# Kernel tuning notes

Hardware: AMD Instinct MI355X
Metric: run time of the kernel (lower is better)

Reference implementation:

```python
import jax, jax.numpy as jnp
import numpy as np

DIM = 64  # per-head dim used for the sqrt scale


def setup_inputs() -> dict:
    key = jax.random.key(0)
    kq, kk, kv, ke, kf = jax.random.split(key, 5)
    B, N, d, k = 32, 4096, 64, 256
    Q = jax.random.normal(kq, (B, N, d), dtype=jnp.float32)
    K = jax.random.normal(kk, (B, N, d), dtype=jnp.float32)
    V = jax.random.normal(kv, (B, N, d), dtype=jnp.float32)
    E = jax.random.normal(ke, (N, k), dtype=jnp.float32) * (1.0 / np.sqrt(N))
    F = jax.random.normal(kf, (N, k), dtype=jnp.float32) * (1.0 / np.sqrt(N))
    return {"Q": Q, "K": K, "V": V, "E": E, "F": F}


def reference(Q, K, V, E, F):
    # Linformer head: K^T E -> [B,d,k]; Q (K^T E) / sqrt(d) -> [B,N,k]
    K_proj = jnp.einsum('bnd,nk->bdk', K, E)          # low-rank key projection
    scores = jnp.einsum('bnd,bdk->bnk', Q, K_proj) / jnp.sqrt(jnp.float32(DIM))
    P_bar = jax.nn.softmax(scores, axis=2)            # [B,N,k]
    # (V^T F)^T -> [B,k,d]
    V_proj = jnp.einsum('bnd,nk->bkd', V, F)
    return jnp.einsum('bnk,bkd->bnd', P_bar, V_proj)  # [B,N,d]
```

## Files before the change

### kernel.cpp

```cpp
#include <hip/hip_runtime.h>
#include <hip/hip_bf16.h>

#define BB 32
#define NN 4096
#define DDIM 64
#define KKR 256

typedef __attribute__((ext_vector_type(8)))  short bf16x8;
typedef __attribute__((ext_vector_type(16))) float f32x16;
typedef __attribute__((ext_vector_type(4)))  float f32x4;

static __device__ inline unsigned short f2bf(float x) {
  union { float f; unsigned u; } v; v.f = x;
  unsigned r = (v.u + 0x7FFFu + ((v.u >> 16) & 1u)) >> 16;
  return (unsigned short)r;
}

__global__ __launch_bounds__(256) void pass0_kernel(
    const float* __restrict__ Q, const float* __restrict__ K,
    const float* __restrict__ V, const float* __restrict__ E,
    const float* __restrict__ F,
    unsigned short* __restrict__ Qb, unsigned short* __restrict__ KT,
    unsigned short* __restrict__ VT, unsigned short* __restrict__ ET,
    unsigned short* __restrict__ FT)
{
  __shared__ unsigned short T[64 * 72];
  const int id = blockIdx.x;
  const int t  = threadIdx.x;

  if (id < 4608) {
    const float* src; unsigned short* dst; int srcStride, row0, col0;
    if (id < 2048) {
      int b = id >> 6, nt = id & 63;
      src = K + (long)b * NN * DDIM; dst = KT + (long)b * DDIM * NN;
      srcStride = 64; row0 = nt * 64; col0 = 0;
    } else if (id < 4096) {
      int i2 = id - 2048; int b = i2 >> 6, nt = i2 & 63;
      src = V + (long)b * NN * DDIM; dst = VT + (long)b * DDIM * NN;
      srcStride = 64; row0 = nt * 64; col0 = 0;
    } else if (id < 4352) {
      int i2 = id - 4096; int nt = i2 >> 2, ct = i2 & 3;
      src = E; dst = ET; srcStride = 256; row0 = nt * 64; col0 = ct * 64;
    } else {
      int i2 = id - 4352; int nt = i2 >> 2, ct = i2 & 3;
      src = F; dst = FT; srcStride = 256; row0 = nt * 64; col0 = ct * 64;
    }
    const int r  = t >> 2;
    const int cq = t & 3;
    const float* sp = src + (long)(row0 + r) * srcStride + col0 + cq * 16;
    float4 v0 = *(const float4*)(sp + 0);
    float4 v1 = *(const float4*)(sp + 4);
    float4 v2 = *(const float4*)(sp + 8);
    float4 v3 = *(const float4*)(sp + 12);
    const int cb = cq * 16;
    T[(cb + 0)  * 72 + r] = f2bf(v0.x);  T[(cb + 1)  * 72 + r] = f2bf(v0.y);
    T[(cb + 2)  * 72 + r] = f2bf(v0.z);  T[(cb + 3)  * 72 + r] = f2bf(v0.w);
    T[(cb + 4)  * 72 + r] = f2bf(v1.x);  T[(cb + 5)  * 72 + r] = f2bf(v1.y);
    T[(cb + 6)  * 72 + r] = f2bf(v1.z);  T[(cb + 7)  * 72 + r] = f2bf(v1.w);
    T[(cb + 8)  * 72 + r] = f2bf(v2.x);  T[(cb + 9)  * 72 + r] = f2bf(v2.y);
    T[(cb + 10) * 72 + r] = f2bf(v2.z);  T[(cb + 11) * 72 + r] = f2bf(v2.w);
    T[(cb + 12) * 72 + r] = f2bf(v3.x);  T[(cb + 13) * 72 + r] = f2bf(v3.y);
    T[(cb + 14) * 72 + r] = f2bf(v3.z);  T[(cb + 15) * 72 + r] = f2bf(v3.w);
    __syncthreads();
    const int cf = t >> 2;
    const int no = (t & 3) * 16;
    bf16x8 o0 = *(const bf16x8*)&T[cf * 72 + no];
    bf16x8 o1 = *(const bf16x8*)&T[cf * 72 + no + 8];
    unsigned short* dp = dst + (long)(col0 + cf) * NN + row0 + no;
    *(bf16x8*)dp       = o0;
    *(bf16x8*)(dp + 8) = o1;
  } else {
    const long base = (long)(id - 4608) * 4096 + t * 16;
    float4 a = *(const float4*)(Q + base + 0);
    float4 b = *(const float4*)(Q + base + 4);
    float4 c = *(const float4*)(Q + base + 8);
    float4 d = *(const float4*)(Q + base + 12);
    unsigned short o[16];
    o[0]=f2bf(a.x); o[1]=f2bf(a.y); o[2]=f2bf(a.z); o[3]=f2bf(a.w);
    o[4]=f2bf(b.x); o[5]=f2bf(b.y); o[6]=f2bf(b.z); o[7]=f2bf(b.w);
    o[8]=f2bf(c.x); o[9]=f2bf(c.y); o[10]=f2bf(c.z); o[11]=f2bf(c.w);
    o[12]=f2bf(d.x); o[13]=f2bf(d.y); o[14]=f2bf(d.z); o[15]=f2bf(d.w);
    *(bf16x8*)(Qb + base)     = *(const bf16x8*)&o[0];
    *(bf16x8*)(Qb + base + 8) = *(const bf16x8*)&o[8];
  }
}

__global__ __launch_bounds__(256, 2) void proj_gemm(
    const unsigned short* __restrict__ KT, const unsigned short* __restrict__ VT,
    const unsigned short* __restrict__ ET, const unsigned short* __restrict__ FT,
    float* __restrict__ KpA, float* __restrict__ VpA)
{
  extern __shared__ unsigned short sm[];
  const int blk = blockIdx.x;
  const int chunk = blk & 7, mat = (blk >> 3) & 1, b = blk >> 4;
  const int t = threadIdx.x, w = t >> 6, l = t & 63, h = l >> 5, lr = l & 31;

  const unsigned short *Ag, *Bg; int M; float* Cg;
  if (mat == 0) { Ag = ET; Bg = KT + (long)b * DDIM * NN; M = 256; Cg = KpA + b * 16384; }
  else          { Ag = VT + (long)b * DDIM * NN; Bg = FT; M = 64;  Cg = VpA + b * 16384; }
  const int mt0 = (mat == 0) ? 2 * w : 0;
  const int nt0 = (mat == 0) ? 0 : 2 * w;

  f32x16 acc[2][2];
#pragma unroll
  for (int i = 0; i < 2; ++i)
#pragma unroll
    for (int j = 0; j < 2; ++j)
#pragma unroll
      for (int q = 0; q < 16; ++q) acc[i][j][q] = 0.f;

  const int n0 = chunk * 512;
  for (int stg = 0; stg < 8; ++stg) {
    const int nb = n0 + stg * 64;
    __syncthreads();
#pragma unroll
    for (int i = 0; i < 10; ++i) {
      int c = i * 256 + t;
      int row = c >> 3, off = c & 7;
      const unsigned short* g =
          (row < M ? Ag + (long)row * NN : Bg + (long)(row - M) * NN) + nb + off * 8;
      *(bf16x8*)&sm[row * 72 + off * 8] = *(const bf16x8*)g;
    }
    __syncthreads();
#pragma unroll
    for (int kk = 0; kk < 4; ++kk) {
      bf16x8 a0 = *(const bf16x8*)&sm[(mt0 * 32 + lr) * 72 + kk * 16 + h * 8];
      bf16x8 a1 = *(const bf16x8*)&sm[((mt0 + 1) * 32 + lr) * 72 + kk * 16 + h * 8];
      bf16x8 b0 = *(const bf16x8*)&sm[(M + nt0 * 32 + lr) * 72 + kk * 16 + h * 8];
      bf16x8 b1 = *(const bf16x8*)&sm[(M + (nt0 + 1) * 32 + lr) * 72 + kk * 16 + h * 8];
      acc[0][0] = __builtin_amdgcn_mfma_f32_32x32x16_bf16(a0, b0, acc[0][0], 0, 0, 0);
      acc[0][1] = __builtin_amdgcn_mfma_f32_32x32x16_bf16(a0, b1, acc[0][1], 0, 0, 0);
      acc[1][0] = __builtin_amdgcn_mfma_f32_32x32x16_bf16(a1, b0, acc[1][0], 0, 0, 0);
      acc[1][1] = __builtin_amdgcn_mfma_f32_32x32x16_bf16(a1, b1, acc[1][1], 0, 0, 0);
    }
  }
#pragma unroll
  for (int mt = 0; mt < 2; ++mt)
#pragma unroll
    for (int nt = 0; nt < 2; ++nt)
#pragma unroll
      for (int i = 0; i < 16; ++i) {
        int row = (mt0 + mt) * 32 + (i & 3) + 8 * (i >> 2) + 4 * h;
        int col = (nt0 + nt) * 32 + lr;
        int idx = (mat == 0) ? row * 64 + col : row * 256 + col;
        unsafeAtomicAdd(&Cg[idx], acc[mt][nt][i]);
      }
}

__global__ __launch_bounds__(256) void cvt_kernel(
    const float* __restrict__ src, unsigned short* __restrict__ dst)
{
  const long i = ((long)blockIdx.x * 256 + threadIdx.x) * 8;
  float4 a = *(const float4*)(src + i);
  float4 b = *(const float4*)(src + i + 4);
  unsigned short o[8];
  o[0]=f2bf(a.x); o[1]=f2bf(a.y); o[2]=f2bf(a.z); o[3]=f2bf(a.w);
  o[4]=f2bf(b.x); o[5]=f2bf(b.y); o[6]=f2bf(b.z); o[7]=f2bf(b.w);
  *(bf16x8*)(dst + i) = *(const bf16x8*)&o[0];
}

__global__ __launch_bounds__(256, 2) void attn2_kernel(
    const unsigned short* __restrict__ Qb, const unsigned short* __restrict__ Kpb,
    const unsigned short* __restrict__ Vpb, float* __restrict__ Og)
{
  extern __shared__ char smraw[];
  unsigned short* P = (unsigned short*)smraw;
  float* scr = (float*)(smraw + 65536);
  float* red = (float*)(smraw + 65536 + 8192);

  const int blk = blockIdx.x;
  const int b = blk >> 5, rg = blk & 31;
  const int t = threadIdx.x, w = t >> 6, l = t & 63, h = l >> 5, lr = l & 31;
  const int rh = w >> 1, ch = w & 1;

  const unsigned short* Qbase = Qb + ((long)b * NN + rg * 128) * 64;
  bf16x8 A[2][4];
#pragma unroll
  for (int rt = 0; rt < 2; ++rt)
#pragma unroll
    for (int kk = 0; kk < 4; ++kk)
      A[rt][kk] = *(const bf16x8*)(Qbase + (long)(rh * 64 + rt * 32 + lr) * 64 + kk * 16 + h * 8);

  const unsigned short* Kp = Kpb + (long)b * 16384;
  f32x16 acc[2][4];
#pragma unroll
  for (int rt = 0; rt < 2; ++rt)
#pragma unroll
    for (int ct = 0; ct < 4; ++ct)
#pragma unroll
      for (int q = 0; q < 16; ++q) acc[rt][ct][q] = 0.f;

  bf16x8 Bf[4], Bn[4];
#pragma unroll
  for (int ct = 0; ct < 4; ++ct)
    Bf[ct] = *(const bf16x8*)(Kp + (long)(ch * 128 + ct * 32 + lr) * 64 + h * 8);
#pragma unroll
  for (int kk = 0; kk < 4; ++kk) {
    if (kk < 3) {
#pragma unroll
      for (int ct = 0; ct < 4; ++ct)
        Bn[ct] = *(const bf16x8*)(Kp + (long)(ch * 128 + ct * 32 + lr) * 64 + (kk + 1) * 16 + h * 8);
    }
#pragma unroll
    for (int ct = 0; ct < 4; ++ct) {
      acc[0][ct] = __builtin_amdgcn_mfma_f32_32x32x16_bf16(A[0][kk], Bf[ct], acc[0][ct], 0, 0, 0);
      acc[1][ct] = __builtin_amdgcn_mfma_f32_32x32x16_bf16(A[1][kk], Bf[ct], acc[1][ct], 0, 0, 0);
    }
#pragma unroll
    for (int ct = 0; ct < 4; ++ct) Bf[ct] = Bn[ct];
  }

#pragma unroll
  for (int rt = 0; rt < 2; ++rt)
#pragma unroll
    for (int ct = 0; ct < 4; ++ct)
#pragma unroll
      for (int q = 0; q < 16; ++q)
        acc[rt][ct][q] = __expf(acc[rt][ct][q] * 0.125f);

  float ps[2][16];
#pragma unroll
  for (int rt = 0; rt < 2; ++rt)
#pragma unroll
    for (int q = 0; q < 16; ++q)
      ps[rt][q] = (acc[rt][0][q] + acc[rt][1][q]) + (acc[rt][2][q] + acc[rt][3][q]);
#pragma unroll
  for (int rt = 0; rt < 2; ++rt)
#pragma unroll
    for (int q = 0; q < 16; ++q) {
      ps[rt][q] += __shfl_xor(ps[rt][q], 8);
      ps[rt][q] += __shfl_xor(ps[rt][q], 16);
    }
  if (((l >> 3) & 3) == 0) {
#pragma unroll
    for (int rt = 0; rt < 2; ++rt)
#pragma unroll
      for (int q = 0; q < 16; ++q) {
        int rowL = (q & 3) + 8 * (q >> 2) + 4 * h;
        scr[w * 512 + (rt * 32 + rowL) * 8 + (l & 7)] = ps[rt][q];
      }
  }
  {
    const float* p = &scr[w * 512 + l * 8];
    f32x4 x = *(const f32x4*)p, y = *(const f32x4*)(p + 4);
    float s = (x[0] + x[1]) + (x[2] + x[3]) + (y[0] + y[1]) + (y[2] + y[3]);
    red[ch * 128 + rh * 64 + l] = s;
  }

#pragma unroll
  for (int rt = 0; rt < 2; ++rt)
#pragma unroll
    for (int ct = 0; ct < 4; ++ct)
#pragma unroll
      for (int q = 0; q < 16; ++q) {
        int rowL = rh * 64 + rt * 32 + (q & 3) + 8 * (q >> 2) + 4 * h;
        int col  = ch * 128 + ct * 32 + lr;
        int chk  = (col >> 3) ^ (rowL & 7);
        P[rowL * 256 + chk * 8 + (col & 7)] = f2bf(acc[rt][ct][q]);
      }
  __syncthreads();

  const unsigned short* Vp = Vpb + (long)b * 16384;
  f32x16 o[2];
#pragma unroll
  for (int rt = 0; rt < 2; ++rt)
#pragma unroll
    for (int q = 0; q < 16; ++q) o[rt][q] = 0.f;

#pragma unroll
  for (int kk = 0; kk < 16; ++kk) {
    bf16x8 Bv = *(const bf16x8*)(Vp + (long)(ch * 32 + lr) * 256 + kk * 16 + h * 8);
    bf16x8 Ap[2];
#pragma unroll
    for (int rt = 0; rt < 2; ++rt) {
      int rowL = rh * 64 + rt * 32 + lr;
      int col  = kk * 16 + h * 8;
      int chk  = (col >> 3) ^ (rowL & 7);
      Ap[rt] = *(const bf16x8*)&P[rowL * 256 + chk * 8];
    }
    o[0] = __builtin_amdgcn_mfma_f32_32x32x16_bf16(Ap[0], Bv, o[0], 0, 0, 0);
    o[1] = __builtin_amdgcn_mfma_f32_32x32x16_bf16(Ap[1], Bv, o[1], 0, 0, 0);
  }

#pragma unroll
  for (int rt = 0; rt < 2; ++rt)
#pragma unroll
    for (int ig = 0; ig < 4; ++ig) {
      int r0 = rh * 64 + rt * 32 + ig * 8 + 4 * h;
      f32x4 l0 = *(const f32x4*)&red[r0];
      f32x4 l1 = *(const f32x4*)&red[128 + r0];
#pragma unroll
      for (int j = 0; j < 4; ++j) {
        float val = o[rt][ig * 4 + j] / (l0[j] + l1[j]);
        Og[((long)b * NN + rg * 128 + r0 + j) * 64 + ch * 32 + lr] = val;
      }
    }
}

extern "C" void kernel_launch(void* const* d_in, const int* in_sizes, int n_in,
                              void* d_out, int out_size, void* d_ws, size_t ws_size,
                              hipStream_t stream) {
  const float* Q = (const float*)d_in[0];
  const float* K = (const float*)d_in[1];
  const float* V = (const float*)d_in[2];
  const float* E = (const float*)d_in[3];
  const float* F = (const float*)d_in[4];
  float* out = (float*)d_out;

  char* ws = (char*)d_ws;
  float*          KpA = (float*)(ws);
  float*          VpA = (float*)(ws + (2l << 20));
  unsigned short* Kpb = (unsigned short*)(ws + (4l << 20));
  unsigned short* Vpb = (unsigned short*)(ws + (5l << 20));
  unsigned short* Qb  = (unsigned short*)(ws + (6l << 20));
  unsigned short* KT  = (unsigned short*)(ws + (22l << 20));
  unsigned short* VT  = (unsigned short*)(ws + (38l << 20));
  unsigned short* ET  = (unsigned short*)(ws + (54l << 20));
  unsigned short* FT  = (unsigned short*)(ws + (56l << 20));

  hipMemsetAsync(d_ws, 0, (size_t)4 << 20, stream);

  pass0_kernel<<<dim3(6656), dim3(256), 0, stream>>>(Q, K, V, E, F, Qb, KT, VT, ET, FT);

  hipFuncSetAttribute((const void*)proj_gemm,
                      hipFuncAttributeMaxDynamicSharedMemorySize, 46080);
  proj_gemm<<<dim3(512), dim3(256), 46080, stream>>>(KT, VT, ET, FT, KpA, VpA);

  cvt_kernel<<<dim3(512), dim3(256), 0, stream>>>(KpA, Kpb);

  hipFuncSetAttribute((const void*)attn2_kernel,
                      hipFuncAttributeMaxDynamicSharedMemorySize, 74752);
  attn2_kernel<<<dim3(1024), dim3(256), 74752, stream>>>(Qb, Kpb, Vpb, out);
}
```

Before: 230.3 us.

## Fuse Q conversion into attention, replace atomics with partial-sum reduction

Drops the separate Q fp32->bf16 pass and converts Q directly when loading it in the attention kernel, removing a full write and re-read of a Qb buffer. The projection GEMM now uses 4 chunks with plain stores of per-chunk partials, and a new reduce_cvt kernel sums them and converts both Kp and Vp to bf16. This removes the workspace memset and the atomics. pass0's transpose now uses strided scalar loads and direct stores instead of an LDS-staged transpose, which may coalesce worse. exp is switched to exp2 with a prescaled constant and the final division to a reciprocal multiply.

```diff
diff --git a/kernel.cpp b/kernel.cpp
--- a/kernel.cpp
+++ b/kernel.cpp
@@ -17,87 +17,62 @@
 }
 
 __global__ __launch_bounds__(256) void pass0_kernel(
-    const float* __restrict__ Q, const float* __restrict__ K,
-    const float* __restrict__ V, const float* __restrict__ E,
-    const float* __restrict__ F,
-    unsigned short* __restrict__ Qb, unsigned short* __restrict__ KT,
-    unsigned short* __restrict__ VT, unsigned short* __restrict__ ET,
-    unsigned short* __restrict__ FT)
+    const float* __restrict__ K, const float* __restrict__ V,
+    const float* __restrict__ E, const float* __restrict__ F,
+    unsigned short* __restrict__ KT, unsigned short* __restrict__ VT,
+    unsigned short* __restrict__ ET, unsigned short* __restrict__ FT)
 {
-  __shared__ unsigned short T[64 * 72];
   const int id = blockIdx.x;
   const int t  = threadIdx.x;
-
-  if (id < 4608) {
-    const float* src; unsigned short* dst; int srcStride, row0, col0;
-    if (id < 2048) {
-      int b = id >> 6, nt = id & 63;
-      src = K + (long)b * NN * DDIM; dst = KT + (long)b * DDIM * NN;
-      srcStride = 64; row0 = nt * 64; col0 = 0;
-    } else if (id < 4096) {
-      int i2 = id - 2048; int b = i2 >> 6, nt = i2 & 63;
-      src = V + (long)b * NN * DDIM; dst = VT + (long)b * DDIM * NN;
-      srcStride = 64; row0 = nt * 64; col0 = 0;
-    } else if (id < 4352) {
-      int i2 = id - 4096; int nt = i2 >> 2, ct = i2 & 3;
-      src = E; dst = ET; srcStride = 256; row0 = nt * 64; col0 = ct * 64;
-    } else {
-      int i2 = id - 4352; int nt = i2 >> 2, ct = i2 & 3;
-      src = F; dst = FT; srcStride = 256; row0 = nt * 64; col0 = ct * 64;
-    }
-    const int r  = t >> 2;
-    const int cq = t & 3;
-    const float* sp = src + (long)(row0 + r) * srcStride + col0 + cq * 16;
-    float4 v0 = *(const float4*)(sp + 0);
-    float4 v1 = *(const float4*)(sp + 4);
-    float4 v2 = *(const float4*)(sp + 8);
-    float4 v3 = *(const float4*)(sp + 12);
-    const int cb = cq * 16;
-    T[(cb + 0)  * 72 + r] = f2bf(v0.x);  T[(cb + 1)  * 72 + r] = f2bf(v0.y);
-    T[(cb + 2)  * 72 + r] = f2bf(v0.z);  T[(cb + 3)  * 72 + r] = f2bf(v0.w);
-    T[(cb + 4)  * 72 + r] = f2bf(v1.x);  T[(cb + 5)  * 72 + r] = f2bf(v1.y);
-    T[(cb + 6)  * 72 + r] = f2bf(v1.z);  T[(cb + 7)  * 72 + r] = f2bf(v1.w);
-    T[(cb + 8)  * 72 + r] = f2bf(v2.x);  T[(cb + 9)  * 72 + r] = f2bf(v2.y);
-    T[(cb + 10) * 72 + r] = f2bf(v2.z);  T[(cb + 11) * 72 + r] = f2bf(v2.w);
-    T[(cb + 12) * 72 + r] = f2bf(v3.x);  T[(cb + 13) * 72 + r] = f2bf(v3.y);
-    T[(cb + 14) * 72 + r] = f2bf(v3.z);  T[(cb + 15) * 72 + r] = f2bf(v3.w);
-    __syncthreads();
-    const int cf = t >> 2;
-    const int no = (t & 3) * 16;
-    bf16x8 o0 = *(const bf16x8*)&T[cf * 72 + no];
-    bf16x8 o1 = *(const bf16x8*)&T[cf * 72 + no + 8];
-    unsigned short* dp = dst + (long)(col0 + cf) * NN + row0 + no;
-    *(bf16x8*)dp       = o0;
-    *(bf16x8*)(dp + 8) = o1;
+  const float* src; unsigned short* dst; int stride, n0, col0;
+  if (id < 2048) {
+    int b = id >> 6, nt = id & 63;
+    src = K + (long)b * NN * DDIM; dst = KT + (long)b * DDIM * NN;
+    stride = 64; n0 = nt * 64; col0 = 0;
+  } else if (id < 4096) {
+    int i2 = id - 2048; int b = i2 >> 6, nt = i2 & 63;
+    src = V + (long)b * NN * DDIM; dst = VT + (long)b * DDIM * NN;
+    stride = 64; n0 = nt * 64; col0 = 0;
+  } else if (id < 4352) {
+    int i2 = id - 4096; int nt = i2 >> 2, ct = i2 & 3;
+    src = E; dst = ET; stride = 256; n0 = nt * 64; col0 = ct * 64;
   } else {
-    const long base = (long)(id - 4608) * 4096 + t * 16;
-    float4 a = *(const float4*)(Q + base + 0);
-    float4 b = *(const float4*)(Q + base + 4);
-    float4 c = *(const float4*)(Q + base + 8);
-    float4 d = *(const float4*)(Q + base + 12);
-    unsigned short o[16];
-    o[0]=f2bf(a.x); o[1]=f2bf(a.y); o[2]=f2bf(a.z); o[3]=f2bf(a.w);
-    o[4]=f2bf(b.x); o[5]=f2bf(b.y); o[6]=f2bf(b.z); o[7]=f2bf(b.w);
-    o[8]=f2bf(c.x); o[9]=f2bf(c.y); o[10]=f2bf(c.z); o[11]=f2bf(c.w);
-    o[12]=f2bf(d.x); o[13]=f2bf(d.y); o[14]=f2bf(d.z); o[15]=f2bf(d.w);
-    *(bf16x8*)(Qb + base)     = *(const bf16x8*)&o[0];
-    *(bf16x8*)(Qb + base + 8) = *(const bf16x8*)&o[8];
-  }
+    int i2 = id - 4352; int nt = i2 >> 2, ct = i2 & 3;
+    src = F; dst = FT; stride = 256; n0 = nt * 64; col0 = ct * 64;
+  }
+  const int c = t & 63;
+  const int q = t >> 6;
+  const float* sp = src + (long)(n0 + q * 16) * stride + col0 + c;
+  float v[16];
+#pragma unroll
+  for (int j = 0; j < 16; ++j) v[j] = sp[(long)j * stride];
+  unsigned short o[16];
+#pragma unroll
+  for (int j = 0; j < 16; ++j) o[j] = f2bf(v[j]);
+  unsigned short* dp = dst + (long)(col0 + c) * NN + n0 + q * 16;
+#pragma unroll
+  for (int j4 = 0; j4 < 4; ++j4)
+    *(ushort4*)(dp + j4 * 4) = *(const ushort4*)&o[j4 * 4];
 }
 
 __global__ __launch_bounds__(256, 2) void proj_gemm(
     const unsigned short* __restrict__ KT, const unsigned short* __restrict__ VT,
     const unsigned short* __restrict__ ET, const unsigned short* __restrict__ FT,
-    float* __restrict__ KpA, float* __restrict__ VpA)
+    float* __restrict__ KpP, float* __restrict__ VpP)
 {
   extern __shared__ unsigned short sm[];
   const int blk = blockIdx.x;
-  const int chunk = blk & 7, mat = (blk >> 3) & 1, b = blk >> 4;
+  const int chunk = blk & 3, mat = (blk >> 2) & 1, b = blk >> 3;
   const int t = threadIdx.x, w = t >> 6, l = t & 63, h = l >> 5, lr = l & 31;
 
   const unsigned short *Ag, *Bg; int M; float* Cg;
-  if (mat == 0) { Ag = ET; Bg = KT + (long)b * DDIM * NN; M = 256; Cg = KpA + b * 16384; }
-  else          { Ag = VT + (long)b * DDIM * NN; Bg = FT; M = 64;  Cg = VpA + b * 16384; }
+  if (mat == 0) {
+    Ag = ET; Bg = KT + (long)b * DDIM * NN; M = 256;
+    Cg = KpP + (long)chunk * (BB * 16384) + b * 16384;
+  } else {
+    Ag = VT + (long)b * DDIM * NN; Bg = FT; M = 64;
+    Cg = VpP + (long)chunk * (BB * 16384) + b * 16384;
+  }
   const int mt0 = (mat == 0) ? 2 * w : 0;
   const int nt0 = (mat == 0) ? 0 : 2 * w;
 
@@ -109,14 +84,14 @@
 #pragma unroll
       for (int q = 0; q < 16; ++q) acc[i][j][q] = 0.f;
 
-  const int n0 = chunk * 512;
-  for (int stg = 0; stg < 8; ++stg) {
+  const int n0 = chunk * 1024;
+  for (int stg = 0; stg < 16; ++stg) {
     const int nb = n0 + stg * 64;
     __syncthreads();
 #pragma unroll
     for (int i = 0; i < 10; ++i) {
-      int c = i * 256 + t;
-      int row = c >> 3, off = c & 7;
+      int cidx = i * 256 + t;
+      int row = cidx >> 3, off = cidx & 7;
       const unsigned short* g =
           (row < M ? Ag + (long)row * NN : Bg + (long)(row - M) * NN) + nb + off * 8;
       *(bf16x8*)&sm[row * 72 + off * 8] = *(const bf16x8*)g;
@@ -143,24 +118,36 @@
         int row = (mt0 + mt) * 32 + (i & 3) + 8 * (i >> 2) + 4 * h;
         int col = (nt0 + nt) * 32 + lr;
         int idx = (mat == 0) ? row * 64 + col : row * 256 + col;
-        unsafeAtomicAdd(&Cg[idx], acc[mt][nt][i]);
+        Cg[idx] = acc[mt][nt][i];
       }
 }
 
-__global__ __launch_bounds__(256) void cvt_kernel(
-    const float* __restrict__ src, unsigned short* __restrict__ dst)
+__global__ __launch_bounds__(256) void reduce_cvt(
+    const float* __restrict__ KpP, const float* __restrict__ VpP,
+    unsigned short* __restrict__ Kpb, unsigned short* __restrict__ Vpb)
 {
-  const long i = ((long)blockIdx.x * 256 + threadIdx.x) * 8;
-  float4 a = *(const float4*)(src + i);
-  float4 b = *(const float4*)(src + i + 4);
+  const int blk = blockIdx.x;
+  const float* src = (blk < 256) ? KpP : VpP;
+  unsigned short* dst = (blk < 256) ? Kpb : Vpb;
+  const long i = (long)(blk & 255) * 2048 + threadIdx.x * 8;
+  float a[8];
+#pragma unroll
+  for (int j = 0; j < 8; ++j) a[j] = 0.f;
+#pragma unroll
+  for (int cch = 0; cch < 4; ++cch) {
+    const float4 p0 = *(const float4*)(src + (long)cch * (BB * 16384) + i);
+    const float4 p1 = *(const float4*)(src + (long)cch * (BB * 16384) + i + 4);
+    a[0] += p0.x; a[1] += p0.y; a[2] += p0.z; a[3] += p0.w;
+    a[4] += p1.x; a[5] += p1.y; a[6] += p1.z; a[7] += p1.w;
+  }
   unsigned short o[8];
-  o[0]=f2bf(a.x); o[1]=f2bf(a.y); o[2]=f2bf(a.z); o[3]=f2bf(a.w);
-  o[4]=f2bf(b.x); o[5]=f2bf(b.y); o[6]=f2bf(b.z); o[7]=f2bf(b.w);
+#pragma unroll
+  for (int j = 0; j < 8; ++j) o[j] = f2bf(a[j]);
   *(bf16x8*)(dst + i) = *(const bf16x8*)&o[0];
 }
 
 __global__ __launch_bounds__(256, 2) void attn2_kernel(
-    const unsigned short* __restrict__ Qb, const unsigned short* __restrict__ Kpb,
+    const float* __restrict__ Qg, const unsigned short* __restrict__ Kpb,
     const unsigned short* __restrict__ Vpb, float* __restrict__ Og)
 {
   extern __shared__ char smraw[];
@@ -173,13 +160,20 @@
   const int t = threadIdx.x, w = t >> 6, l = t & 63, h = l >> 5, lr = l & 31;
   const int rh = w >> 1, ch = w & 1;
 
-  const unsigned short* Qbase = Qb + ((long)b * NN + rg * 128) * 64;
+  const float* Qbase = Qg + ((long)b * NN + rg * 128) * 64;
   bf16x8 A[2][4];
 #pragma unroll
   for (int rt = 0; rt < 2; ++rt)
 #pragma unroll
-    for (int kk = 0; kk < 4; ++kk)
-      A[rt][kk] = *(const bf16x8*)(Qbase + (long)(rh * 64 + rt * 32 + lr) * 64 + kk * 16 + h * 8);
+    for (int kk = 0; kk < 4; ++kk) {
+      const float* qp = Qbase + (long)(rh * 64 + rt * 32 + lr) * 64 + kk * 16 + h * 8;
+      float4 x = *(const float4*)qp;
+      float4 y = *(const float4*)(qp + 4);
+      unsigned short u[8];
+      u[0] = f2bf(x.x); u[1] = f2bf(x.y); u[2] = f2bf(x.z); u[3] = f2bf(x.w);
+      u[4] = f2bf(y.x); u[5] = f2bf(y.y); u[6] = f2bf(y.z); u[7] = f2bf(y.w);
+      A[rt][kk] = *(const bf16x8*)u;
+    }
 
   const unsigned short* Kp = Kpb + (long)b * 16384;
   f32x16 acc[2][4];
@@ -216,7 +210,7 @@
     for (int ct = 0; ct < 4; ++ct)
 #pragma unroll
       for (int q = 0; q < 16; ++q)
-        acc[rt][ct][q] = __expf(acc[rt][ct][q] * 0.125f);
+        acc[rt][ct][q] = exp2f(acc[rt][ct][q] * 0.1803368801f);
 
   float ps[2][16];
 #pragma unroll
@@ -291,7 +285,7 @@
       f32x4 l1 = *(const f32x4*)&red[128 + r0];
 #pragma unroll
       for (int j = 0; j < 4; ++j) {
-        float val = o[rt][ig * 4 + j] / (l0[j] + l1[j]);
+        float val = o[rt][ig * 4 + j] * __builtin_amdgcn_rcpf(l0[j] + l1[j]);
         Og[((long)b * NN + rg * 128 + r0 + j) * 64 + ch * 32 + lr] = val;
       }
     }
@@ -308,27 +302,24 @@
   float* out = (float*)d_out;
 
   char* ws = (char*)d_ws;
-  float*          KpA = (float*)(ws);
-  float*          VpA = (float*)(ws + (2l << 20));
-  unsigned short* Kpb = (unsigned short*)(ws + (4l << 20));
-  unsigned short* Vpb = (unsigned short*)(ws + (5l << 20));
-  unsigned short* Qb  = (unsigned short*)(ws + (6l << 20));
-  unsigned short* KT  = (unsigned short*)(ws + (22l << 20));
-  unsigned short* VT  = (unsigned short*)(ws + (38l << 20));
-  unsigned short* ET  = (unsigned short*)(ws + (54l << 20));
-  unsigned short* FT  = (unsigned short*)(ws + (56l << 20));
-
-  hipMemsetAsync(d_ws, 0, (size_t)4 << 20, stream);
-
-  pass0_kernel<<<dim3(6656), dim3(256), 0, stream>>>(Q, K, V, E, F, Qb, KT, VT, ET, FT);
+  float*          KpP = (float*)(ws);
+  float*          VpP = (float*)(ws + (8l << 20));
+  unsigned short* Kpb = (unsigned short*)(ws + (16l << 20));
+  unsigned short* Vpb = (unsigned short*)(ws + (17l << 20));
+  unsigned short* KT  = (unsigned short*)(ws + (18l << 20));
+  unsigned short* VT  = (unsigned short*)(ws + (34l << 20));
+  unsigned short* ET  = (unsigned short*)(ws + (50l << 20));
+  unsigned short* FT  = (unsigned short*)(ws + (52l << 20));
+
+  pass0_kernel<<<dim3(4608), dim3(256), 0, stream>>>(K, V, E, F, KT, VT, ET, FT);
 
   hipFuncSetAttribute((const void*)proj_gemm,
                       hipFuncAttributeMaxDynamicSharedMemorySize, 46080);
-  proj_gemm<<<dim3(512), dim3(256), 46080, stream>>>(KT, VT, ET, FT, KpA, VpA);
-
-  cvt_kernel<<<dim3(512), dim3(256), 0, stream>>>(KpA, Kpb);
+  proj_gemm<<<dim3(256), dim3(256), 46080, stream>>>(KT, VT, ET, FT, KpP, VpP);
+
+  reduce_cvt<<<dim3(512), dim3(256), 0, stream>>>(KpP, VpP, Kpb, Vpb);
 
   hipFuncSetAttribute((const void*)attn2_kernel,
                       hipFuncAttributeMaxDynamicSharedMemorySize, 74752);
-  attn2_kernel<<<dim3(1024), dim3(256), 74752, stream>>>(Qb, Kpb, Vpb, out);
-}
+  attn2_kernel<<<dim3(1024), dim3(256), 74752, stream>>>(Q, Kpb, Vpb, out);
+}
```

Result: faster. 214.2 us (-7.0%).
